# Kernel tuning notes

Measured on AMD Instinct MI355X. Metric: run time of the kernel, lower is better.

The kernel has to match this reference:

```python
import jax, jax.numpy as jnp
import numpy as np

H, W = 480, 640
NUM_CLASSES = 3
SKIP = 5            # skip_pixels: stride between voting pixels
GRID = 8            # stride of Hough accumulator bins
LABEL_THRESHOLD = 5
INLIER_THRESHOLD = 0.5
VOTING_THRESHOLD = 0.3


def setup_inputs():
    key = jax.random.key(0)
    k1, k2, k3, k4 = jax.random.split(key, 4)
    bottom_label = jax.random.randint(k1, (1, H, W), 0, NUM_CLASSES).astype(jnp.int32)
    bottom_vertex = jax.random.normal(k2, (1, NUM_CLASSES * 3, H, W), jnp.float32)
    bottom_meta_data = jax.random.normal(k3, (1, 10), jnp.float32)
    extents = jax.random.normal(k4, (NUM_CLASSES, 3), jnp.float32)
    return {"bottom_label": bottom_label, "bottom_vertex": bottom_vertex,
            "bottom_meta_data": bottom_meta_data, "extents": extents}


def _hough_voting(bottom_label, bottom_vertex, bottom_meta_data, extents):
    label = bottom_label[0]                                   # [H,W] int
    vert = bottom_vertex[0].reshape(NUM_CLASSES, 3, H, W)     # per-class (ux,uy,dist)

    # voter pixels on a SKIP-strided grid
    vy, vx = jnp.meshgrid(jnp.arange(0, H, SKIP), jnp.arange(0, W, SKIP), indexing="ij")
    vy = vy.reshape(-1)
    vx = vx.reshape(-1)                                       # [V]
    vl = label[vy, vx]                                        # voter class labels [V]
    d = vert[vl, :, vy, vx]                                   # [V,3] gather own-class prediction
    ux, uy, dist = d[:, 0], d[:, 1], d[:, 2]

    # Hough bin centers on a GRID-strided grid
    by, bx = jnp.meshgrid(jnp.arange(GRID // 2, H, GRID), jnp.arange(GRID // 2, W, GRID), indexing="ij")
    by = by.reshape(-1).astype(jnp.float32)
    bx = bx.reshape(-1).astype(jnp.float32)                   # [B]

    # per (voter, bin) agreement between predicted direction and vector to bin
    ddx = bx[None, :] - vx[:, None].astype(jnp.float32)       # [V,B]
    ddy = by[None, :] - vy[:, None].astype(jnp.float32)
    inv_n = jax.lax.rsqrt(ddx * ddx + ddy * ddy + 1e-6)
    cos = (ddx * ux[:, None] + ddy * uy[:, None]) * inv_n     # [V,B]
    w = jnp.where((cos > INLIER_THRESHOLD) & (vl[:, None] > 0), 1.0, 0.0)

    # scatter votes into per-class Hough space (class 0 = background, masked above)
    hough = jax.ops.segment_sum(w, vl, num_segments=NUM_CLASSES)                 # [C,B]
    dsum = jax.ops.segment_sum(w * dist[:, None], vl, num_segments=NUM_CLASSES)  # [C,B]
    counts = jax.ops.segment_sum(jnp.ones_like(vl, jnp.float32), vl, num_segments=NUM_CLASSES)

    # peak detection per class
    peak = jnp.argmax(hough, axis=1)                          # [C]
    votes = jnp.take_along_axis(hough, peak[:, None], axis=1)[:, 0]
    depth = jnp.take_along_axis(dsum, peak[:, None], axis=1)[:, 0] / jnp.maximum(votes, 1.0)
    cx = bx[peak]
    cy = by[peak]
    score = votes / jnp.maximum(counts, 1.0)
    valid = (counts > LABEL_THRESHOLD) & (score > VOTING_THRESHOLD)

    # project object extents through camera intrinsics at estimated depth -> box size
    fx = bottom_meta_data[0, 0]
    fy = bottom_meta_data[0, 4]
    diag = jnp.sqrt(jnp.sum(extents * extents, axis=1))       # [C]
    safe_z = jnp.maximum(jnp.abs(depth), 1e-3)
    bw = jnp.abs(diag * fx) / safe_z
    bh = jnp.abs(diag * fy) / safe_z

    cls = jnp.arange(NUM_CLASSES, dtype=jnp.float32)
    rois = jnp.stack([cls, cx - bw / 2, cy - bh / 2, cx + bw / 2, cy + bh / 2,
                      score * valid.astype(jnp.float32)], axis=1)  # [C,6]
    return rois, hough


def reference(bottom_label, bottom_vertex, bottom_meta_data, extents):
    return _hough_voting(bottom_label, bottom_vertex, bottom_meta_data, extents)
```

## Files before the change

kernel.cpp:

```cpp
#include <hip/hip_runtime.h>

#define HH 480
#define WW 640
#define NC 3
#define NVX 128
#define NVY 96
#define NV (NVX * NVY)
#define NBX 80
#define NBY 60
#define NB (NBX * NBY)
#define NPB 48
#define BINBLOCKS ((NB + 255) / 256)

__global__ void precompute_pts(const int* __restrict__ label,
                               const float* __restrict__ vert,
                               float4* __restrict__ ptsA,
                               float4* __restrict__ ptsB,
                               int* __restrict__ cnt,
                               float* __restrict__ blockCounts,
                               float* __restrict__ hough,
                               float* __restrict__ dsum) {
    __shared__ int swtot[4], sn2[4];
    const int tid = threadIdx.x;
    const int i = blockIdx.x * 256 + tid;
    const int iy = i >> 7;
    const int ix = i & (NVX - 1);
    const int pix = (5 * iy) * WW + 5 * ix;
    const int vl = label[pix];
    const float* base = vert + (size_t)(vl * 3) * HH * WW + pix;
    const float ux = base[0];
    const float uy = base[(size_t)HH * WW];
    const float dist = base[(size_t)2 * HH * WW];

    const bool pos = (vl > 0);
    const int lane = tid & 63, w = tid >> 6;
    unsigned long long mp = __ballot(pos);
    unsigned long long m2 = __ballot(vl == 2);
    int rank = __popcll(mp & ((1ull << lane) - 1ull));
    if (lane == 0) { swtot[w] = __popcll(mp); sn2[w] = __popcll(m2); }
    __syncthreads();
    int off = 0;
    for (int k = 0; k < w; ++k) off += swtot[k];
    if (pos) {
        int p = blockIdx.x * 256 + off + rank;
        ptsA[p] = make_float4((float)(5 * ix), (float)(5 * iy), ux, uy);
        float c2 = (vl == 2) ? 1.0f : 0.0f;
        ptsB[p] = make_float4((vl == 1) ? dist : 0.0f,
                              (vl == 2) ? dist : 0.0f,
                              (vl == 1) ? 1.0f : 0.0f, c2);
    }
    if (tid == 0) {
        int tot = swtot[0] + swtot[1] + swtot[2] + swtot[3];
        int n2 = sn2[0] + sn2[1] + sn2[2] + sn2[3];
        cnt[blockIdx.x] = tot;
        blockCounts[blockIdx.x * NC + 0] = (float)(256 - tot);
        blockCounts[blockIdx.x * NC + 1] = (float)(tot - n2);
        blockCounts[blockIdx.x * NC + 2] = (float)n2;
    }
    for (int k = i; k < NC * NB; k += NV) hough[k] = 0.0f;
    if (i < 2 * NB) dsum[i] = 0.0f;
}

__global__ void vote(const float4* __restrict__ ptsA,
                     const float4* __restrict__ ptsB,
                     const int* __restrict__ cnt,
                     float* __restrict__ hough,
                     float* __restrict__ dsum) {
    __shared__ float4 shA[256];
    __shared__ float4 shB[256];
    const int tid = threadIdx.x;
    const int p0 = blockIdx.y * 256;
    shA[tid] = ptsA[p0 + tid];
    shB[tid] = ptsB[p0 + tid];
    const int n = cnt[blockIdx.y];

    const int b = blockIdx.x * 256 + tid;
    const float bxf = (float)(4 + 8 * (b % NBX));
    const float byf = (float)(4 + 8 * (b / NBX));
    float h1 = 0.f, h2 = 0.f, d1 = 0.f, d2 = 0.f;
    __syncthreads();

#pragma unroll 4
    for (int j = 0; j < n; ++j) {
        float4 a = shA[j];
        float4 q = shB[j];
        float ddx = bxf - a.x;
        float ddy = byf - a.y;
        float nx  = __builtin_fmaf(ddx, ddx, __builtin_fmaf(ddy, ddy, 1e-6f));
        float dot = __builtin_fmaf(ddx, a.z, ddy * a.w);
        float s   = __builtin_fmaf(dot, dot, -0.25f * nx);
        bool v = (dot > 0.0f) & (s > 0.0f);
        if (__builtin_expect((dot > 0.0f) && (fabsf(s) < nx * 2e-5f), 0)) {
            float nxe  = __fadd_rn(__fadd_rn(__fmul_rn(ddx, ddx),
                                             __fmul_rn(ddy, ddy)), 1e-6f);
            float inve = __fdiv_rn(1.0f, __fsqrt_rn(nxe));
            float dote = __fadd_rn(__fmul_rn(ddx, a.z), __fmul_rn(ddy, a.w));
            v = __fmul_rn(dote, inve) > 0.5f;
        }
        float m = v ? 1.0f : 0.0f;
        d1 = __builtin_fmaf(m, q.x, d1);
        d2 = __builtin_fmaf(m, q.y, d2);
        h1 = __builtin_fmaf(m, q.z, h1);
        h2 = __builtin_fmaf(m, q.w, h2);
    }
    if (b < NB) {
        atomicAdd(&hough[NB + b], h1);
        atomicAdd(&hough[2 * NB + b], h2);
        atomicAdd(&dsum[b], d1);
        atomicAdd(&dsum[NB + b], d2);
    }
}

__global__ void finalize(const float* __restrict__ hough,
                         const float* __restrict__ dsum,
                         const float* __restrict__ blockCounts,
                         const float* __restrict__ meta,
                         const float* __restrict__ extents,
                         float* __restrict__ rois) {
    __shared__ unsigned long long skey[256];
    __shared__ float scnt[256];
    const int tid = threadIdx.x;
    const int c = blockIdx.x;

    float cntv = 0.0f;
    for (int i = tid; i < NPB; i += 256) cntv += blockCounts[i * NC + c];
    scnt[tid] = cntv;

    unsigned long long best = 0ull;
    for (int i = tid; i < NB; i += 256) {
        float v = hough[c * NB + i];
        unsigned long long key =
            ((unsigned long long)__float_as_uint(v) << 32) |
            (unsigned long long)(unsigned)(NB - 1 - i);
        if (key > best) best = key;
    }
    skey[tid] = best;
    __syncthreads();
    for (int s = 128; s > 0; s >>= 1) {
        if (tid < s) {
            if (skey[tid + s] > skey[tid]) skey[tid] = skey[tid + s];
            scnt[tid] += scnt[tid + s];
        }
        __syncthreads();
    }
    if (tid == 0) {
        float votes = __uint_as_float((unsigned)(skey[0] >> 32));
        int peak = NB - 1 - (int)(skey[0] & 0xffffffffull);
        float ds = (c == 0) ? 0.0f : dsum[(c - 1) * NB + peak];
        float depth = __fdiv_rn(ds, fmaxf(votes, 1.0f));
        float cx = (float)(4 + 8 * (peak % NBX));
        float cy = (float)(4 + 8 * (peak / NBX));
        float cntf = scnt[0];
        float score = __fdiv_rn(votes, fmaxf(cntf, 1.0f));
        int valid = (cntf > 5.0f) && (score > 0.3f);
        float fx = meta[0], fy = meta[4];
        float e0 = extents[c * 3 + 0];
        float e1 = extents[c * 3 + 1];
        float e2 = extents[c * 3 + 2];
        float diag = __fsqrt_rn(__fadd_rn(
            __fadd_rn(__fmul_rn(e0, e0), __fmul_rn(e1, e1)), __fmul_rn(e2, e2)));
        float sz = fmaxf(fabsf(depth), 0.001f);
        float bw = __fdiv_rn(fabsf(__fmul_rn(diag, fx)), sz);
        float bh = __fdiv_rn(fabsf(__fmul_rn(diag, fy)), sz);
        rois[c * 6 + 0] = (float)c;
        rois[c * 6 + 1] = cx - bw * 0.5f;
        rois[c * 6 + 2] = cy - bh * 0.5f;
        rois[c * 6 + 3] = cx + bw * 0.5f;
        rois[c * 6 + 4] = cy + bh * 0.5f;
        rois[c * 6 + 5] = valid ? score : 0.0f;
    }
}

extern "C" void kernel_launch(void* const* d_in, const int* in_sizes, int n_in,
                              void* d_out, int out_size, void* d_ws, size_t ws_size,
                              hipStream_t stream) {
    const int* label = (const int*)d_in[0];
    const float* vert = (const float*)d_in[1];
    const float* meta = (const float*)d_in[2];
    const float* extents = (const float*)d_in[3];
    float* out = (float*)d_out;

    char* ws = (char*)d_ws;
    float4* ptsA = (float4*)ws;
    float4* ptsB = (float4*)(ws + (size_t)NV * 16);
    float* dsum = (float*)(ws + (size_t)2 * NV * 16);
    float* blockCounts = (float*)(ws + (size_t)2 * NV * 16 + 2 * NB * 4);
    int* cnt = (int*)(ws + (size_t)2 * NV * 16 + 2 * NB * 4 + NPB * NC * 4);

    float* hough = out + NC * 6;

    precompute_pts<<<NPB, 256, 0, stream>>>(label, vert, ptsA, ptsB,
                                            cnt, blockCounts, hough, dsum);
    vote<<<dim3(BINBLOCKS, NPB), 256, 0, stream>>>(ptsA, ptsB, cnt, hough, dsum);
    finalize<<<NC, 256, 0, stream>>>(hough, dsum, blockCounts, meta, extents, out);
}
```

Measured before the change: 98.36 us.

## Fuse voter compaction into vote kernel and replace atomics with slice-partial reduction

Each vote block now reads labels and vertex data directly and compacts the class-1 and class-2 voters into shared memory, which removes the separate precompute kernel and its global point buffers. The inner loop is split into two class-specific loops, so each pair costs one accumulator update plus one depth FMA instead of four FMAs. Float atomics are replaced by per-slice partial writes, which a new reduce kernel sums deterministically while also computing per-block argmax candidates; a single-warp finalize then does the rest. The price is that each of the 19 bin blocks per slice repeats the label and vertex gather, and the partial buffer adds extra global traffic.

```diff
diff --git a/kernel.cpp b/kernel.cpp
--- a/kernel.cpp
+++ b/kernel.cpp
@@ -2,6 +2,7 @@
 
 #define HH 480
 #define WW 640
+#define HW (HH * WW)
 #define NC 3
 #define NVX 128
 #define NVY 96
@@ -9,159 +10,174 @@
 #define NBX 80
 #define NBY 60
 #define NB (NBX * NBY)
-#define NPB 48
+#define NSL 48
 #define BINBLOCKS ((NB + 255) / 256)
 
-__global__ void precompute_pts(const int* __restrict__ label,
-                               const float* __restrict__ vert,
-                               float4* __restrict__ ptsA,
-                               float4* __restrict__ ptsB,
-                               int* __restrict__ cnt,
-                               float* __restrict__ blockCounts,
-                               float* __restrict__ hough,
-                               float* __restrict__ dsum) {
-    __shared__ int swtot[4], sn2[4];
+__global__ void vote_fused(const int* __restrict__ label,
+                           const float* __restrict__ vert,
+                           float4* __restrict__ partial,
+                           int2* __restrict__ sliceCounts) {
+    __shared__ float4 shA[256];
+    __shared__ float  shD[256];
+    __shared__ int sw1[4], sw2[4];
+
     const int tid = threadIdx.x;
-    const int i = blockIdx.x * 256 + tid;
+    const int slice = blockIdx.y;
+    const int i = slice * 256 + tid;
     const int iy = i >> 7;
     const int ix = i & (NVX - 1);
     const int pix = (5 * iy) * WW + 5 * ix;
     const int vl = label[pix];
-    const float* base = vert + (size_t)(vl * 3) * HH * WW + pix;
+    const float* base = vert + (size_t)(vl * 3) * HW + pix;
     const float ux = base[0];
-    const float uy = base[(size_t)HH * WW];
-    const float dist = base[(size_t)2 * HH * WW];
-
-    const bool pos = (vl > 0);
+    const float uy = base[HW];
+    const float dist = base[(size_t)2 * HW];
+
     const int lane = tid & 63, w = tid >> 6;
-    unsigned long long mp = __ballot(pos);
-    unsigned long long m2 = __ballot(vl == 2);
-    int rank = __popcll(mp & ((1ull << lane) - 1ull));
-    if (lane == 0) { swtot[w] = __popcll(mp); sn2[w] = __popcll(m2); }
+    const unsigned long long lt = (1ull << lane) - 1ull;
+    const unsigned long long m1 = __ballot(vl == 1);
+    const unsigned long long m2 = __ballot(vl == 2);
+    if (lane == 0) { sw1[w] = __popcll(m1); sw2[w] = __popcll(m2); }
     __syncthreads();
-    int off = 0;
-    for (int k = 0; k < w; ++k) off += swtot[k];
-    if (pos) {
-        int p = blockIdx.x * 256 + off + rank;
-        ptsA[p] = make_float4((float)(5 * ix), (float)(5 * iy), ux, uy);
-        float c2 = (vl == 2) ? 1.0f : 0.0f;
-        ptsB[p] = make_float4((vl == 1) ? dist : 0.0f,
-                              (vl == 2) ? dist : 0.0f,
-                              (vl == 1) ? 1.0f : 0.0f, c2);
-    }
-    if (tid == 0) {
-        int tot = swtot[0] + swtot[1] + swtot[2] + swtot[3];
-        int n2 = sn2[0] + sn2[1] + sn2[2] + sn2[3];
-        cnt[blockIdx.x] = tot;
-        blockCounts[blockIdx.x * NC + 0] = (float)(256 - tot);
-        blockCounts[blockIdx.x * NC + 1] = (float)(tot - n2);
-        blockCounts[blockIdx.x * NC + 2] = (float)n2;
-    }
-    for (int k = i; k < NC * NB; k += NV) hough[k] = 0.0f;
-    if (i < 2 * NB) dsum[i] = 0.0f;
-}
-
-__global__ void vote(const float4* __restrict__ ptsA,
-                     const float4* __restrict__ ptsB,
-                     const int* __restrict__ cnt,
-                     float* __restrict__ hough,
-                     float* __restrict__ dsum) {
-    __shared__ float4 shA[256];
-    __shared__ float4 shB[256];
-    const int tid = threadIdx.x;
-    const int p0 = blockIdx.y * 256;
-    shA[tid] = ptsA[p0 + tid];
-    shB[tid] = ptsB[p0 + tid];
-    const int n = cnt[blockIdx.y];
+    const int n1 = sw1[0] + sw1[1] + sw1[2] + sw1[3];
+    const int n2 = sw2[0] + sw2[1] + sw2[2] + sw2[3];
+    int o1 = 0, o2 = 0;
+    for (int k = 0; k < w; ++k) { o1 += sw1[k]; o2 += sw2[k]; }
+    if (vl == 1) {
+        int p = o1 + __popcll(m1 & lt);
+        shA[p] = make_float4((float)(5 * ix), (float)(5 * iy), 2.0f * ux, 2.0f * uy);
+        shD[p] = dist;
+    } else if (vl == 2) {
+        int p = n1 + o2 + __popcll(m2 & lt);
+        shA[p] = make_float4((float)(5 * ix), (float)(5 * iy), 2.0f * ux, 2.0f * uy);
+        shD[p] = dist;
+    }
+    if (blockIdx.x == 0 && tid == 0) sliceCounts[slice] = make_int2(n1, n2);
+    __syncthreads();
 
     const int b = blockIdx.x * 256 + tid;
     const float bxf = (float)(4 + 8 * (b % NBX));
     const float byf = (float)(4 + 8 * (b / NBX));
-    float h1 = 0.f, h2 = 0.f, d1 = 0.f, d2 = 0.f;
+    float h1 = 0.f, d1 = 0.f, h2 = 0.f, d2 = 0.f;
+
+    const int e1 = __builtin_amdgcn_readfirstlane(n1);
+    const int e2 = __builtin_amdgcn_readfirstlane(n1 + n2);
+
+#define PAIR_BODY(HACC, DACC)                                                        \
+    {                                                                                \
+        float4 a = shA[j];                                                           \
+        float ddx = bxf - a.x;                                                       \
+        float ddy = byf - a.y;                                                       \
+        float nx  = __builtin_fmaf(ddx, ddx, __builtin_fmaf(ddy, ddy, 1e-6f));       \
+        float dot = __builtin_fmaf(ddx, a.z, ddy * a.w);                             \
+        float s   = __builtin_fmaf(dot, dot, -nx);                                   \
+        bool v = (dot > 0.0f) & (s > 0.0f);                                          \
+        if (__builtin_expect((dot > 0.0f) && (fabsf(s) < nx * 8e-5f), 0)) {          \
+            float nxe  = __fadd_rn(__fadd_rn(__fmul_rn(ddx, ddx),                    \
+                                             __fmul_rn(ddy, ddy)), 1e-6f);           \
+            float inve = __fdiv_rn(1.0f, __fsqrt_rn(nxe));                           \
+            float dote = __fadd_rn(__fmul_rn(ddx, 0.5f * a.z),                       \
+                                   __fmul_rn(ddy, 0.5f * a.w));                      \
+            v = __fmul_rn(dote, inve) > 0.5f;                                        \
+        }                                                                            \
+        float m = v ? 1.0f : 0.0f;                                                   \
+        HACC += m;                                                                   \
+        DACC = __builtin_fmaf(m, shD[j], DACC);                                      \
+    }
+
+#pragma unroll 4
+    for (int j = 0; j < e1; ++j) PAIR_BODY(h1, d1)
+#pragma unroll 4
+    for (int j = e1; j < e2; ++j) PAIR_BODY(h2, d2)
+#undef PAIR_BODY
+
+    if (b < NB) partial[slice * NB + b] = make_float4(h1, d1, h2, d2);
+}
+
+__global__ void reduce_vote(const float4* __restrict__ partial,
+                            float* __restrict__ hough,
+                            float* __restrict__ dsum,
+                            unsigned long long* __restrict__ cand) {
+    __shared__ unsigned long long sk1[256], sk2[256];
+    const int tid = threadIdx.x;
+    const int b = blockIdx.x * 256 + tid;
+    unsigned long long k1 = 0ull, k2 = 0ull;
+    if (b < NB) {
+        float h1 = 0.f, d1 = 0.f, h2 = 0.f, d2 = 0.f;
+#pragma unroll 8
+        for (int s = 0; s < NSL; ++s) {
+            float4 p = partial[s * NB + b];
+            h1 += p.x; d1 += p.y; h2 += p.z; d2 += p.w;
+        }
+        hough[b] = 0.0f;
+        hough[NB + b] = h1;
+        hough[2 * NB + b] = h2;
+        dsum[b] = d1;
+        dsum[NB + b] = d2;
+        const unsigned long long idx = (unsigned long long)(unsigned)(NB - 1 - b);
+        k1 = ((unsigned long long)__float_as_uint(h1) << 32) | idx;
+        k2 = ((unsigned long long)__float_as_uint(h2) << 32) | idx;
+    }
+    sk1[tid] = k1; sk2[tid] = k2;
     __syncthreads();
-
-#pragma unroll 4
-    for (int j = 0; j < n; ++j) {
-        float4 a = shA[j];
-        float4 q = shB[j];
-        float ddx = bxf - a.x;
-        float ddy = byf - a.y;
-        float nx  = __builtin_fmaf(ddx, ddx, __builtin_fmaf(ddy, ddy, 1e-6f));
-        float dot = __builtin_fmaf(ddx, a.z, ddy * a.w);
-        float s   = __builtin_fmaf(dot, dot, -0.25f * nx);
-        bool v = (dot > 0.0f) & (s > 0.0f);
-        if (__builtin_expect((dot > 0.0f) && (fabsf(s) < nx * 2e-5f), 0)) {
-            float nxe  = __fadd_rn(__fadd_rn(__fmul_rn(ddx, ddx),
-                                             __fmul_rn(ddy, ddy)), 1e-6f);
-            float inve = __fdiv_rn(1.0f, __fsqrt_rn(nxe));
-            float dote = __fadd_rn(__fmul_rn(ddx, a.z), __fmul_rn(ddy, a.w));
-            v = __fmul_rn(dote, inve) > 0.5f;
+    for (int s = 128; s > 0; s >>= 1) {
+        if (tid < s) {
+            if (sk1[tid + s] > sk1[tid]) sk1[tid] = sk1[tid + s];
+            if (sk2[tid + s] > sk2[tid]) sk2[tid] = sk2[tid + s];
         }
-        float m = v ? 1.0f : 0.0f;
-        d1 = __builtin_fmaf(m, q.x, d1);
-        d2 = __builtin_fmaf(m, q.y, d2);
-        h1 = __builtin_fmaf(m, q.z, h1);
-        h2 = __builtin_fmaf(m, q.w, h2);
-    }
-    if (b < NB) {
-        atomicAdd(&hough[NB + b], h1);
-        atomicAdd(&hough[2 * NB + b], h2);
-        atomicAdd(&dsum[b], d1);
-        atomicAdd(&dsum[NB + b], d2);
-    }
-}
-
-__global__ void finalize(const float* __restrict__ hough,
+        __syncthreads();
+    }
+    if (tid == 0) {
+        cand[blockIdx.x * 2]     = sk1[0];
+        cand[blockIdx.x * 2 + 1] = sk2[0];
+    }
+}
+
+__global__ void finalize(const unsigned long long* __restrict__ cand,
+                         const int2* __restrict__ sliceCounts,
                          const float* __restrict__ dsum,
-                         const float* __restrict__ blockCounts,
                          const float* __restrict__ meta,
                          const float* __restrict__ extents,
                          float* __restrict__ rois) {
-    __shared__ unsigned long long skey[256];
-    __shared__ float scnt[256];
     const int tid = threadIdx.x;
-    const int c = blockIdx.x;
-
-    float cntv = 0.0f;
-    for (int i = tid; i < NPB; i += 256) cntv += blockCounts[i * NC + c];
-    scnt[tid] = cntv;
-
-    unsigned long long best = 0ull;
-    for (int i = tid; i < NB; i += 256) {
-        float v = hough[c * NB + i];
-        unsigned long long key =
-            ((unsigned long long)__float_as_uint(v) << 32) |
-            (unsigned long long)(unsigned)(NB - 1 - i);
-        if (key > best) best = key;
-    }
-    skey[tid] = best;
-    __syncthreads();
-    for (int s = 128; s > 0; s >>= 1) {
-        if (tid < s) {
-            if (skey[tid + s] > skey[tid]) skey[tid] = skey[tid + s];
-            scnt[tid] += scnt[tid + s];
+    unsigned long long k1 = (tid < BINBLOCKS) ? cand[tid * 2]     : 0ull;
+    unsigned long long k2 = (tid < BINBLOCKS) ? cand[tid * 2 + 1] : 0ull;
+    int cn1 = 0, cn2 = 0;
+    if (tid < NSL) { int2 c = sliceCounts[tid]; cn1 = c.x; cn2 = c.y; }
+    for (int off = 32; off > 0; off >>= 1) {
+        unsigned long long o1 = __shfl_xor(k1, off);
+        unsigned long long o2 = __shfl_xor(k2, off);
+        if (o1 > k1) k1 = o1;
+        if (o2 > k2) k2 = o2;
+        cn1 += __shfl_xor(cn1, off);
+        cn2 += __shfl_xor(cn2, off);
+    }
+    if (tid < NC) {
+        const int c = tid;
+        float votes; int peak;
+        if (c == 0) { votes = 0.0f; peak = 0; }
+        else {
+            unsigned long long k = (c == 1) ? k1 : k2;
+            votes = __uint_as_float((unsigned)(k >> 32));
+            peak = NB - 1 - (int)(k & 0xffffffffull);
         }
-        __syncthreads();
-    }
-    if (tid == 0) {
-        float votes = __uint_as_float((unsigned)(skey[0] >> 32));
-        int peak = NB - 1 - (int)(skey[0] & 0xffffffffull);
-        float ds = (c == 0) ? 0.0f : dsum[(c - 1) * NB + peak];
-        float depth = __fdiv_rn(ds, fmaxf(votes, 1.0f));
-        float cx = (float)(4 + 8 * (peak % NBX));
-        float cy = (float)(4 + 8 * (peak / NBX));
-        float cntf = scnt[0];
-        float score = __fdiv_rn(votes, fmaxf(cntf, 1.0f));
-        int valid = (cntf > 5.0f) && (score > 0.3f);
-        float fx = meta[0], fy = meta[4];
-        float e0 = extents[c * 3 + 0];
-        float e1 = extents[c * 3 + 1];
-        float e2 = extents[c * 3 + 2];
-        float diag = __fsqrt_rn(__fadd_rn(
+        const float cntf = (c == 0) ? (float)(NV - cn1 - cn2)
+                                    : ((c == 1) ? (float)cn1 : (float)cn2);
+        const float ds = (c == 0) ? 0.0f : dsum[(c - 1) * NB + peak];
+        const float depth = __fdiv_rn(ds, fmaxf(votes, 1.0f));
+        const float cx = (float)(4 + 8 * (peak % NBX));
+        const float cy = (float)(4 + 8 * (peak / NBX));
+        const float score = __fdiv_rn(votes, fmaxf(cntf, 1.0f));
+        const int valid = (cntf > 5.0f) && (score > 0.3f);
+        const float fx = meta[0], fy = meta[4];
+        const float e0 = extents[c * 3 + 0];
+        const float e1 = extents[c * 3 + 1];
+        const float e2 = extents[c * 3 + 2];
+        const float diag = __fsqrt_rn(__fadd_rn(
             __fadd_rn(__fmul_rn(e0, e0), __fmul_rn(e1, e1)), __fmul_rn(e2, e2)));
-        float sz = fmaxf(fabsf(depth), 0.001f);
-        float bw = __fdiv_rn(fabsf(__fmul_rn(diag, fx)), sz);
-        float bh = __fdiv_rn(fabsf(__fmul_rn(diag, fy)), sz);
+        const float sz = fmaxf(fabsf(depth), 0.001f);
+        const float bw = __fdiv_rn(fabsf(__fmul_rn(diag, fx)), sz);
+        const float bh = __fdiv_rn(fabsf(__fmul_rn(diag, fy)), sz);
         rois[c * 6 + 0] = (float)c;
         rois[c * 6 + 1] = cx - bw * 0.5f;
         rois[c * 6 + 2] = cy - bh * 0.5f;
@@ -181,16 +197,16 @@
     float* out = (float*)d_out;
 
     char* ws = (char*)d_ws;
-    float4* ptsA = (float4*)ws;
-    float4* ptsB = (float4*)(ws + (size_t)NV * 16);
-    float* dsum = (float*)(ws + (size_t)2 * NV * 16);
-    float* blockCounts = (float*)(ws + (size_t)2 * NV * 16 + 2 * NB * 4);
-    int* cnt = (int*)(ws + (size_t)2 * NV * 16 + 2 * NB * 4 + NPB * NC * 4);
+    float4* partial = (float4*)ws;
+    float* dsum = (float*)(ws + (size_t)NSL * NB * 16);
+    unsigned long long* cand =
+        (unsigned long long*)(ws + (size_t)NSL * NB * 16 + 2 * NB * 4);
+    int2* sliceCounts =
+        (int2*)(ws + (size_t)NSL * NB * 16 + 2 * NB * 4 + 2 * BINBLOCKS * 8);
 
     float* hough = out + NC * 6;
 
-    precompute_pts<<<NPB, 256, 0, stream>>>(label, vert, ptsA, ptsB,
-                                            cnt, blockCounts, hough, dsum);
-    vote<<<dim3(BINBLOCKS, NPB), 256, 0, stream>>>(ptsA, ptsB, cnt, hough, dsum);
-    finalize<<<NC, 256, 0, stream>>>(hough, dsum, blockCounts, meta, extents, out);
-}
+    vote_fused<<<dim3(BINBLOCKS, NSL), 256, 0, stream>>>(label, vert, partial, sliceCounts);
+    reduce_vote<<<BINBLOCKS, 256, 0, stream>>>(partial, hough, dsum, cand);
+    finalize<<<1, 64, 0, stream>>>(cand, sliceCounts, dsum, meta, extents, out);
+}
```

Measured after the change: 97.96 us. No clear change (-0.4%).
